# Kernel tuning notes

Hardware: AMD Instinct MI355X
Metric: run time of the kernel (lower is better)

## Reference

```python
import jax, jax.numpy as jnp
import numpy as np

B, D, CTX, H = 8192, 64, 256, 512  # batch, latent dim (made.nin), context dim, MADE hidden


def _masks(D, H):
    """Standard MADE natural-ordering masks (Germain et al. 2015)."""
    m0 = np.arange(1, D + 1)                 # input degrees 1..D
    mh = (np.arange(H) % (D - 1)) + 1        # hidden degrees 1..D-1
    M1 = (mh[:, None] >= m0[None, :]).astype(np.float32)   # (H, D)
    M2 = (mh[:, None] >= mh[None, :]).astype(np.float32)   # (H, H)
    mo = np.concatenate([m0, m0])            # outputs = [means; pre_scales]
    Mo = (mo[:, None] > mh[None, :]).astype(np.float32)    # (2D, H)
    return jnp.asarray(M1), jnp.asarray(M2), jnp.asarray(Mo)


def setup_inputs() -> dict:
    key = jax.random.key(0)
    ks = jax.random.split(key, 7)
    s = 0.05
    return {
        "context": jax.random.normal(ks[0], (B, CTX), jnp.float32),
        "eps": jax.random.normal(ks[1], (B, D), jnp.float32),  # reparameterization noise
        "W1": jax.random.normal(ks[2], (H, D), jnp.float32) * s,
        "b1": jnp.zeros((H,), jnp.float32),
        "Wc": jax.random.normal(ks[3], (H, CTX), jnp.float32) * s,
        "W2": jax.random.normal(ks[4], (H, H), jnp.float32) * s,
        "b2": jnp.zeros((H,), jnp.float32),
        "Wo": jax.random.normal(ks[5], (2 * D, H), jnp.float32) * s,
        "bo": jnp.zeros((2 * D,), jnp.float32),
    }


def reference(context, eps, W1, b1, Wc, W2, b2, Wo, bo):
    """AutoRegressiveDistribution.rsample (gaussian): D sequential MADE forwards,
    each extracting column i of (mu, softplus(pre_scale)) and sampling z_i."""
    M1, M2, Mo = _masks(D, H)
    W1m, W2m, Wom = (W1 * M1).T, (W2 * M2).T, (Wo * Mo).T
    ctx_h = context @ Wc.T  # context projection is constant across steps

    def step(z, i):
        h = jax.nn.relu(z @ W1m + ctx_h + b1)   # (B, H)
        h = jax.nn.relu(h @ W2m + b2)           # (B, H)
        out = h @ Wom + bo                      # (B, 2D): [means | pre_scales]
        mu_i = out[:, i]
        scale_i = jax.nn.softplus(out[:, D + i])
        z_i = mu_i + scale_i * eps[:, i]        # Normal(mu, scale).rsample()
        z = z.at[:, i].set(z_i)
        return z, (mu_i, scale_i)

    z0 = jnp.zeros((context.shape[0], D), context.dtype)
    z, (mus, scales) = jax.lax.scan(step, z0, jnp.arange(D))
    # state = (z_sample, mu_inferred, scale_inferred), each (B, D)
    return z, mus.T, scales.T
```

## Files before the change

### kernel.cpp

```cpp
#include <hip/hip_runtime.h>
#include <math.h>


typedef float f2 __attribute__((ext_vector_type(2)));

#define Bn 8192
#define Dn 64
#define CTXn 256
#define Hn 512
#define Rn 16

#define WQ_SZ  (64 * 512 * 12)
#define WOQ_SZ (64 * 64 * 20)
#define WCP_SZ (CTXn * Hn)

#define BARRIER() do {                                      \
    asm volatile("s_waitcnt lgkmcnt(0)" ::: "memory");      \
    __builtin_amdgcn_s_barrier();                           \
    asm volatile("" ::: "memory");                          \
  } while (0)

__device__ __forceinline__ int perm_of(int p, int* degout) {
  int k, t;
  if (p < 72) { k = p / 9 + 1; t = p - (k - 1) * 9; }
  else        { int pp = p - 72; k = pp / 8 + 9; t = pp - (k - 9) * 8; }
  *degout = k;
  return (k - 1) + 63 * t;
}
__device__ __forceinline__ int inv_perm(int h) {
  int i = h % 63;
  int t = h / 63;
  int base = (i < 9) ? 9 * i : 72 + 8 * (i - 8);
  return base + t;
}

#define R0e 262144
#define R1e (R0e + 32768)
#define R2e (R1e + 65536)
#define R3e (R2e + 131072)
#define R4e (R3e + 35840)
#define R5e (R4e + 1024)
__global__ void prep_kernel(const float* __restrict__ W1, const float* __restrict__ Wc,
                            const float* __restrict__ W2, const float* __restrict__ Wo,
                            const float* __restrict__ b1, const float* __restrict__ b2,
                            float* __restrict__ Wq, float* __restrict__ Woq,
                            float* __restrict__ WcpT, float* __restrict__ b1p,
                            float* __restrict__ b2p) {
  int idx = blockIdx.x * 256 + threadIdx.x;
  if (idx < R0e) {
    int hq = idx >> 9, hp = idx & 511;
    int i = hp % 63, e = hp / 63;
    Wq[i * 6144 + inv_perm(hq) * 12 + e] = W2[idx];
  } else if (idx < R1e) {
    int jj = idx - R0e;
    int hq = jj >> 6, i = jj & 63;
    Wq[i * 6144 + inv_perm(hq) * 12 + 9] = W1[jj];
  } else if (idx < R2e) {
    int jj = idx - R1e;
    int o = jj >> 9, hp = jj & 511;
    int i = hp % 63, p = hp / 63;
    int j = o & 63, half = o >> 6;
    Woq[i * 1280 + j * 20 + half * 10 + p] = Wo[jj];
  } else if (idx < R3e) {
    int jj = idx - R2e;
    int hq = jj >> 8, cc = jj & 255;
    int p = inv_perm(hq);
    int slot = (p < 256) ? (2 * p) : (2 * (p - 256) + 1);
    WcpT[cc * 512 + slot] = Wc[jj];
  } else if (idx < R4e) {
    int z = idx - R3e;
    if (z < 28672) {
      int i = 8 + (z >> 9), q = z & 511;
      Wq[i * 6144 + q * 12 + 8] = 0.f;
    } else {
      int z2 = z - 28672;
      int i = 8 + (z2 >> 7), r = z2 & 127;
      int j = r & 63, half = r >> 6;
      Woq[i * 1280 + j * 20 + half * 10 + 8] = 0.f;
    }
  } else if (idx < R5e) {
    int z = idx - R4e;
    if (z < 512) {
      int dq; int hq = perm_of(z, &dq);
      b1p[z] = b1[hq];
    } else {
      int q = z - 512;
      int dq; int hq = perm_of(q, &dq);
      b2p[q] = b2[hq];
    }
  }
}

__global__ __launch_bounds__(256, 2)
void made_pk_kernel(
    const float* __restrict__ context, const float* __restrict__ WcpT,
    const float* __restrict__ b1p,
    const float* __restrict__ Wq, const float* __restrict__ Woq,
    const float* __restrict__ b2p, const float* __restrict__ bo,
    const float* __restrict__ eps, float* __restrict__ out) {
  __shared__ __align__(16) float ctxR[Rn][264];
  __shared__ __align__(16) float zcur[16];
  __shared__ __align__(16) float h1g[9][16];
  __shared__ __align__(16) float h2g[9][16];

  int t = threadIdx.x;
  int b0 = blockIdx.x * Rn;
  int rp = t >> 6, l = t & 63;
  int q0 = t, q1 = t + 256;

  int g0 = ((q0 < 72) ? q0 / 9 + 1 : (q0 - 72) / 8 + 9) - 1;
  int g1 = ((q1 - 72) / 8 + 9) - 1;
  int qm = t | 63;
  int gm0s = __builtin_amdgcn_readfirstlane(
      ((qm < 72) ? qm / 9 + 1 : (qm - 72) / 8 + 9) - 1);
  int gm1s = __builtin_amdgcn_readfirstlane(((qm + 256 - 72) / 8 + 9) - 1);

  #pragma unroll
  for (int r = 0; r < Rn; ++r)
    ctxR[r][t] = context[(b0 + r) * CTXn + t];
  BARRIER();

  f2 accu[16];
  {
    f2 bias = (f2){b1p[q0], b1p[q1]};
    #pragma unroll
    for (int r = 0; r < 16; ++r) accu[r] = bias;
  }
  {
    const float* wc = WcpT + 2 * t;
    #pragma clang loop unroll(disable)
    for (int c4 = 0; c4 < CTXn / 4; ++c4) {
      f2 wv0 = *(const f2*)&wc[0];
      f2 wv1 = *(const f2*)&wc[Hn];
      f2 wv2 = *(const f2*)&wc[2 * Hn];
      f2 wv3 = *(const f2*)&wc[3 * Hn];
      wc += 4 * Hn;
      #pragma unroll
      for (int hf = 0; hf < 2; ++hf) {
        float4 x[8];
        #pragma unroll
        for (int r = 0; r < 8; ++r) x[r] = *(const float4*)&ctxR[8 * hf + r][4 * c4];
        #pragma unroll
        for (int r = 0; r < 8; ++r) {
          accu[8 * hf + r] += (f2){x[r].x, x[r].x} * wv0;
          accu[8 * hf + r] += (f2){x[r].y, x[r].y} * wv1;
          accu[8 * hf + r] += (f2){x[r].z, x[r].z} * wv2;
          accu[8 * hf + r] += (f2){x[r].w, x[r].w} * wv3;
        }
      }
    }
  }

  f2 a10[8], a11[8], a20[8], a21[8];
  #pragma unroll
  for (int r2 = 0; r2 < 8; ++r2) {
    a10[r2] = (f2){accu[2 * r2].x, accu[2 * r2 + 1].x};
    a11[r2] = (f2){accu[2 * r2].y, accu[2 * r2 + 1].y};
  }
  {
    float bb0 = b2p[q0], bb1 = b2p[q1];
    #pragma unroll
    for (int r2 = 0; r2 < 8; ++r2) {
      a20[r2] = (f2){bb0, bb0};
      a21[r2] = (f2){bb1, bb1};
    }
  }

  f2 ocA[2], ocB[2];
  ocA[0] = ocA[1] = (f2){bo[l], bo[l]};
  ocB[0] = ocB[1] = (f2){bo[l + 64], bo[l + 64]};
  int r0 = b0 + 4 * rp;
  f2 ez01 = (f2){eps[(r0 + 0) * Dn + l], eps[(r0 + 1) * Dn + l]};
  f2 ez23 = (f2){eps[(r0 + 2) * Dn + l], eps[(r0 + 3) * Dn + l]};
  f2 zs01 = (f2){0.f, 0.f}, zs23 = zs01;
  f2 mus01 = zs01, mus23 = zs01, scs01 = zs01, scs23 = zs01;

  const float* wq0p = Wq + (size_t)q0 * 12;
  const float* wq1p = Wq + (size_t)q1 * 12;
  const float* wopp = Woq + (size_t)l * 20;

  #pragma clang loop unroll(disable)
  for (int i = 0; i < Dn; ++i) {
    if (l == i) {
      f2 p01 = ocB[0], p23 = ocB[1];
      float s0 = fmaxf(p01.x, 0.f) + __logf(1.f + __expf(-fabsf(p01.x)));
      float s1 = fmaxf(p01.y, 0.f) + __logf(1.f + __expf(-fabsf(p01.y)));
      float s2 = fmaxf(p23.x, 0.f) + __logf(1.f + __expf(-fabsf(p23.x)));
      float s3 = fmaxf(p23.y, 0.f) + __logf(1.f + __expf(-fabsf(p23.y)));
      f2 sc01 = (f2){s0, s1}, sc23 = (f2){s2, s3};
      f2 z01 = ocA[0] + sc01 * ez01;
      f2 z23 = ocA[1] + sc23 * ez23;
      float4 zq = {z01.x, z01.y, z23.x, z23.y};
      *(float4*)&zcur[4 * rp] = zq;
      zs01 = z01; zs23 = z23;
      mus01 = ocA[0]; mus23 = ocA[1];
      scs01 = sc01; scs23 = sc23;
    }
    BARRIER();

    int sb = (i < 8) ? 9 * i : 8 * i + 8;
    bool liveB = (i <= gm1s);
    bool liveA = (i <= gm0s);
    float4 A1c0, A1c1, A1c2, A0c0, A0c1, A0c2;
    if (liveB) {
      const float4* a4 = (const float4*)wq1p;
      A1c0 = a4[0]; A1c1 = a4[1]; A1c2 = a4[2];
      if (liveA) {
        const float4* b4 = (const float4*)wq0p;
        A0c0 = b4[0]; A0c1 = b4[1]; A0c2 = b4[2];
      }
      float4 za = *(const float4*)&zcur[0];
      float4 zb = *(const float4*)&zcur[4];
      float4 zc = *(const float4*)&zcur[8];
      float4 zd = *(const float4*)&zcur[12];
      f2 zz[8] = {(f2){za.x, za.y}, (f2){za.z, za.w},
                  (f2){zb.x, zb.y}, (f2){zb.z, zb.w},
                  (f2){zc.x, zc.y}, (f2){zc.z, zc.w},
                  (f2){zd.x, zd.y}, (f2){zd.z, zd.w}};
      {
        f2 wv = (f2){A1c2.y, A1c2.y};
        #pragma unroll
        for (int r2 = 0; r2 < 8; ++r2) a11[r2] += wv * zz[r2];
        if (g1 == i) {
          int pp = q1 - sb;
          #pragma unroll
          for (int s = 0; s < 4; ++s) {
            float4 h = {fmaxf(a11[2 * s].x, 0.f), fmaxf(a11[2 * s].y, 0.f),
                        fmaxf(a11[2 * s + 1].x, 0.f), fmaxf(a11[2 * s + 1].y, 0.f)};
            *(float4*)&h1g[pp][4 * s] = h;
          }
        }
      }
      if (liveA) {
        f2 wv = (f2){A0c2.y, A0c2.y};
        #pragma unroll
        for (int r2 = 0; r2 < 8; ++r2) a10[r2] += wv * zz[r2];
        if (g0 == i) {
          int pp = q0 - sb;
          #pragma unroll
          for (int s = 0; s < 4; ++s) {
            float4 h = {fmaxf(a10[2 * s].x, 0.f), fmaxf(a10[2 * s].y, 0.f),
                        fmaxf(a10[2 * s + 1].x, 0.f), fmaxf(a10[2 * s + 1].y, 0.f)};
            *(float4*)&h1g[pp][4 * s] = h;
          }
        }
      }
    }
    BARRIER();

    const float4* w4 = (const float4*)wopp;
    float4 B0 = w4[0], B1 = w4[1], B2_ = w4[2], B3 = w4[3], B4 = w4[4];

    if (liveB) {
      float wA1[9] = {A1c0.x, A1c0.y, A1c0.z, A1c0.w,
                      A1c1.x, A1c1.y, A1c1.z, A1c1.w, A1c2.x};
      if (liveA) {
        float wA0[9] = {A0c0.x, A0c0.y, A0c0.z, A0c0.w,
                        A0c1.x, A0c1.y, A0c1.z, A0c1.w, A0c2.x};
        #pragma unroll
        for (int p = 0; p < 9; ++p) {
          float4 ha = *(const float4*)&h1g[p][0];
          float4 hb = *(const float4*)&h1g[p][4];
          float4 hc = *(const float4*)&h1g[p][8];
          float4 hd = *(const float4*)&h1g[p][12];
          f2 h[8] = {(f2){ha.x, ha.y}, (f2){ha.z, ha.w},
                     (f2){hb.x, hb.y}, (f2){hb.z, hb.w},
                     (f2){hc.x, hc.y}, (f2){hc.z, hc.w},
                     (f2){hd.x, hd.y}, (f2){hd.z, hd.w}};
          f2 wv1 = (f2){wA1[p], wA1[p]};
          f2 wv0 = (f2){wA0[p], wA0[p]};
          #pragma unroll
          for (int r2 = 0; r2 < 8; ++r2) {
            a21[r2] += wv1 * h[r2];
            a20[r2] += wv0 * h[r2];
          }
        }
      } else {
        #pragma unroll
        for (int p = 0; p < 9; ++p) {
          float4 ha = *(const float4*)&h1g[p][0];
          float4 hb = *(const float4*)&h1g[p][4];
          float4 hc = *(const float4*)&h1g[p][8];
          float4 hd = *(const float4*)&h1g[p][12];
          f2 h[8] = {(f2){ha.x, ha.y}, (f2){ha.z, ha.w},
                     (f2){hb.x, hb.y}, (f2){hb.z, hb.w},
                     (f2){hc.x, hc.y}, (f2){hc.z, hc.w},
                     (f2){hd.x, hd.y}, (f2){hd.z, hd.w}};
          f2 wv1 = (f2){wA1[p], wA1[p]};
          #pragma unroll
          for (int r2 = 0; r2 < 8; ++r2) a21[r2] += wv1 * h[r2];
        }
      }
      if (g1 == i) {
        int pp = q1 - sb;
        #pragma unroll
        for (int s = 0; s < 4; ++s) {
          float4 h = {fmaxf(a21[2 * s].x, 0.f), fmaxf(a21[2 * s].y, 0.f),
                      fmaxf(a21[2 * s + 1].x, 0.f), fmaxf(a21[2 * s + 1].y, 0.f)};
          *(float4*)&h2g[pp][4 * s] = h;
        }
      }
      if (liveA && g0 == i) {
        int pp = q0 - sb;
        #pragma unroll
        for (int s = 0; s < 4; ++s) {
          float4 h = {fmaxf(a20[2 * s].x, 0.f), fmaxf(a20[2 * s].y, 0.f),
                      fmaxf(a20[2 * s + 1].x, 0.f), fmaxf(a20[2 * s + 1].y, 0.f)};
          *(float4*)&h2g[pp][4 * s] = h;
        }
      }
    }
    BARRIER();

    {
      float wBa[9] = {B0.x, B0.y, B0.z, B0.w, B1.x, B1.y, B1.z, B1.w, B2_.x};
      float wBb[9] = {B2_.z, B2_.w, B3.x, B3.y, B3.z, B3.w, B4.x, B4.y, B4.z};
      #pragma unroll
      for (int p = 0; p < 9; ++p) {
        float4 hq = *(const float4*)&h2g[p][4 * rp];
        f2 h01 = (f2){hq.x, hq.y}, h23 = (f2){hq.z, hq.w};
        f2 wa = (f2){wBa[p], wBa[p]}, wb = (f2){wBb[p], wBb[p]};
        ocA[0] += wa * h01; ocA[1] += wa * h23;
        ocB[0] += wb * h01; ocB[1] += wb * h23;
      }
    }
    wq0p += 6144; wq1p += 6144; wopp += 1280;
  }

  out[(r0 + 0) * Dn + l] = zs01.x;
  out[(r0 + 1) * Dn + l] = zs01.y;
  out[(r0 + 2) * Dn + l] = zs23.x;
  out[(r0 + 3) * Dn + l] = zs23.y;
  out[Bn * Dn + (r0 + 0) * Dn + l] = mus01.x;
  out[Bn * Dn + (r0 + 1) * Dn + l] = mus01.y;
  out[Bn * Dn + (r0 + 2) * Dn + l] = mus23.x;
  out[Bn * Dn + (r0 + 3) * Dn + l] = mus23.y;
  out[2 * Bn * Dn + (r0 + 0) * Dn + l] = scs01.x;
  out[2 * Bn * Dn + (r0 + 1) * Dn + l] = scs01.y;
  out[2 * Bn * Dn + (r0 + 2) * Dn + l] = scs23.x;
  out[2 * Bn * Dn + (r0 + 3) * Dn + l] = scs23.y;
}

extern "C" void kernel_launch(void* const* d_in, const int* in_sizes, int n_in,
                              void* d_out, int out_size, void* d_ws, size_t ws_size,
                              hipStream_t stream) {
  const float* context = (const float*)d_in[0];
  const float* eps     = (const float*)d_in[1];
  const float* W1      = (const float*)d_in[2];
  const float* b1      = (const float*)d_in[3];
  const float* Wc      = (const float*)d_in[4];
  const float* W2      = (const float*)d_in[5];
  const float* b2      = (const float*)d_in[6];
  const float* Wo      = (const float*)d_in[7];
  const float* bo      = (const float*)d_in[8];
  float* out = (float*)d_out;

  float* ws   = (float*)d_ws;
  float* Wq   = ws;
  float* Woq  = Wq + WQ_SZ;
  float* WcpT = Woq + WOQ_SZ;
  float* b1p  = WcpT + WCP_SZ;
  float* b2p  = b1p + 512;

  prep_kernel<<<(R5e + 255) / 256, 256, 0, stream>>>(
      W1, Wc, W2, Wo, b1, b2, Wq, Woq, WcpT, b1p, b2p);
  made_pk_kernel<<<Bn / Rn, 256, 0, stream>>>(context, WcpT, b1p, Wq, Woq,
                                              b2p, bo, eps, out);
}
```

Measured before the change: 237.2 us.

## Software-pipeline MADE step: finish owning group per wave, defer bulk updates a step

```diff
diff --git a/kernel.cpp b/kernel.cpp
--- a/kernel.cpp
+++ b/kernel.cpp
@@ -9,6 +9,7 @@
 #define CTXn 256
 #define Hn 512
 #define Rn 16
+#define BD (Bn * Dn)
 
 #define WQ_SZ  (64 * 512 * 12)
 #define WOQ_SZ (64 * 64 * 20)
@@ -18,6 +19,10 @@
     asm volatile("s_waitcnt lgkmcnt(0)" ::: "memory");      \
     __builtin_amdgcn_s_barrier();                           \
     asm volatile("" ::: "memory");                          \
+  } while (0)
+
+#define WAVE_LDS_FENCE() do {                               \
+    asm volatile("s_waitcnt lgkmcnt(0)" ::: "memory");      \
   } while (0)
 
 __device__ __forceinline__ int perm_of(int p, int* degout) {
@@ -99,9 +104,9 @@
     const float* __restrict__ b2p, const float* __restrict__ bo,
     const float* __restrict__ eps, float* __restrict__ out) {
   __shared__ __align__(16) float ctxR[Rn][264];
-  __shared__ __align__(16) float zcur[16];
-  __shared__ __align__(16) float h1g[9][16];
-  __shared__ __align__(16) float h2g[9][16];
+  __shared__ __align__(16) float zpub[2][16];
+  __shared__ __align__(16) float h1pub[2][9][16];
+  __shared__ __align__(16) float h2pub[2][9][16];
 
   int t = threadIdx.x;
   int b0 = blockIdx.x * Rn;
@@ -150,7 +155,6 @@
       }
     }
   }
-
   f2 a10[8], a11[8], a20[8], a21[8];
   #pragma unroll
   for (int r2 = 0; r2 < 8; ++r2) {
@@ -165,7 +169,6 @@
       a21[r2] = (f2){bb1, bb1};
     }
   }
-
   f2 ocA[2], ocB[2];
   ocA[0] = ocA[1] = (f2){bo[l], bo[l]};
   ocB[0] = ocB[1] = (f2){bo[l + 64], bo[l + 64]};
@@ -175,13 +178,39 @@
   f2 zs01 = (f2){0.f, 0.f}, zs23 = zs01;
   f2 mus01 = zs01, mus23 = zs01, scs01 = zs01, scs23 = zs01;
 
-  const float* wq0p = Wq + (size_t)q0 * 12;
-  const float* wq1p = Wq + (size_t)q1 * 12;
-  const float* wopp = Woq + (size_t)l * 20;
+  float4 C1c0, C1c1, C1c2, C0c0, C0c1, C0c2;
 
   #pragma clang loop unroll(disable)
-  for (int i = 0; i < Dn; ++i) {
-    if (l == i) {
+  for (int S = 0; S < Dn; ++S) {
+    float4 P1c0, P1c1, P1c2, P0c0, P0c1, P0c2;
+    bool pldB = (S <= gm1s);
+    bool pldA = (S <= gm0s);
+    if (pldB) {
+      const float4* a4 = (const float4*)(Wq + (size_t)S * 6144 + (size_t)q1 * 12);
+      P1c0 = a4[0]; P1c1 = a4[1]; P1c2 = a4[2];
+      if (pldA) {
+        const float4* b4 = (const float4*)(Wq + (size_t)S * 6144 + (size_t)q0 * 12);
+        P0c0 = b4[0]; P0c1 = b4[1]; P0c2 = b4[2];
+      }
+    }
+
+    if (S >= 1) {
+      int i = S - 1, pb = i & 1;
+      const float4* w4 = (const float4*)(Woq + (size_t)i * 1280 + (size_t)l * 20);
+      float4 B0 = w4[0], B1 = w4[1], B2_ = w4[2], B3 = w4[3], B4 = w4[4];
+      float wBa[9] = {B0.x, B0.y, B0.z, B0.w, B1.x, B1.y, B1.z, B1.w, B2_.x};
+      float wBb[9] = {B2_.z, B2_.w, B3.x, B3.y, B3.z, B3.w, B4.x, B4.y, B4.z};
+      #pragma unroll
+      for (int p = 0; p < 9; ++p) {
+        float4 hq = *(const float4*)&h2pub[pb][p][4 * rp];
+        f2 h01 = (f2){hq.x, hq.y}, h23 = (f2){hq.z, hq.w};
+        f2 wa = (f2){wBa[p], wBa[p]}, wb = (f2){wBb[p], wBb[p]};
+        ocA[0] += wa * h01; ocA[1] += wa * h23;
+        ocB[0] += wb * h01; ocB[1] += wb * h23;
+      }
+    }
+
+    if (l == S) {
       f2 p01 = ocB[0], p23 = ocB[1];
       float s0 = fmaxf(p01.x, 0.f) + __logf(1.f + __expf(-fabsf(p01.x)));
       float s1 = fmaxf(p01.y, 0.f) + __logf(1.f + __expf(-fabsf(p01.y)));
@@ -190,155 +219,194 @@
       f2 sc01 = (f2){s0, s1}, sc23 = (f2){s2, s3};
       f2 z01 = ocA[0] + sc01 * ez01;
       f2 z23 = ocA[1] + sc23 * ez23;
-      float4 zq = {z01.x, z01.y, z23.x, z23.y};
-      *(float4*)&zcur[4 * rp] = zq;
+      *(float4*)&zpub[S & 1][4 * rp] = (float4){z01.x, z01.y, z23.x, z23.y};
       zs01 = z01; zs23 = z23;
       mus01 = ocA[0]; mus23 = ocA[1];
       scs01 = sc01; scs23 = sc23;
     }
+
+    if (S >= 1) {
+      int i = S - 1, pb = i & 1;
+      bool liveB = (i <= gm1s);
+      bool liveA = (i <= gm0s);
+      if (liveB) {
+        float4 za = *(const float4*)&zpub[pb][0];
+        float4 zb = *(const float4*)&zpub[pb][4];
+        float4 zc = *(const float4*)&zpub[pb][8];
+        float4 zd = *(const float4*)&zpub[pb][12];
+        f2 zz[8] = {(f2){za.x, za.y}, (f2){za.z, za.w},
+                    (f2){zb.x, zb.y}, (f2){zb.z, zb.w},
+                    (f2){zc.x, zc.y}, (f2){zc.z, zc.w},
+                    (f2){zd.x, zd.y}, (f2){zd.z, zd.w}};
+        {
+          f2 wv = (f2){C1c2.y, C1c2.y};
+          #pragma unroll
+          for (int r2 = 0; r2 < 8; ++r2) a11[r2] += wv * zz[r2];
+        }
+        if (liveA) {
+          f2 wv = (f2){C0c2.y, C0c2.y};
+          #pragma unroll
+          for (int r2 = 0; r2 < 8; ++r2) a10[r2] += wv * zz[r2];
+        }
+        float wA1[9] = {C1c0.x, C1c0.y, C1c0.z, C1c0.w,
+                        C1c1.x, C1c1.y, C1c1.z, C1c1.w, C1c2.x};
+        if (liveA) {
+          float wA0[9] = {C0c0.x, C0c0.y, C0c0.z, C0c0.w,
+                          C0c1.x, C0c1.y, C0c1.z, C0c1.w, C0c2.x};
+          #pragma unroll
+          for (int p = 0; p < 9; ++p) {
+            float4 ha = *(const float4*)&h1pub[pb][p][0];
+            float4 hb = *(const float4*)&h1pub[pb][p][4];
+            float4 hc = *(const float4*)&h1pub[pb][p][8];
+            float4 hd = *(const float4*)&h1pub[pb][p][12];
+            f2 h[8] = {(f2){ha.x, ha.y}, (f2){ha.z, ha.w},
+                       (f2){hb.x, hb.y}, (f2){hb.z, hb.w},
+                       (f2){hc.x, hc.y}, (f2){hc.z, hc.w},
+                       (f2){hd.x, hd.y}, (f2){hd.z, hd.w}};
+            f2 wv1 = (f2){wA1[p], wA1[p]};
+            f2 wv0 = (f2){wA0[p], wA0[p]};
+            #pragma unroll
+            for (int r2 = 0; r2 < 8; ++r2) {
+              a21[r2] += wv1 * h[r2];
+              a20[r2] += wv0 * h[r2];
+            }
+          }
+        } else {
+          #pragma unroll
+          for (int p = 0; p < 9; ++p) {
+            float4 ha = *(const float4*)&h1pub[pb][p][0];
+            float4 hb = *(const float4*)&h1pub[pb][p][4];
+            float4 hc = *(const float4*)&h1pub[pb][p][8];
+            float4 hd = *(const float4*)&h1pub[pb][p][12];
+            f2 h[8] = {(f2){ha.x, ha.y}, (f2){ha.z, ha.w},
+                       (f2){hb.x, hb.y}, (f2){hb.z, hb.w},
+                       (f2){hc.x, hc.y}, (f2){hc.z, hc.w},
+                       (f2){hd.x, hd.y}, (f2){hd.z, hd.w}};
+            f2 wv1 = (f2){wA1[p], wA1[p]};
+            #pragma unroll
+            for (int r2 = 0; r2 < 8; ++r2) a21[r2] += wv1 * h[r2];
+          }
+        }
+      }
+    }
     BARRIER();
 
-    int sb = (i < 8) ? 9 * i : 8 * i + 8;
-    bool liveB = (i <= gm1s);
-    bool liveA = (i <= gm0s);
-    float4 A1c0, A1c1, A1c2, A0c0, A0c1, A0c2;
-    if (liveB) {
-      const float4* a4 = (const float4*)wq1p;
-      A1c0 = a4[0]; A1c1 = a4[1]; A1c2 = a4[2];
-      if (liveA) {
-        const float4* b4 = (const float4*)wq0p;
-        A0c0 = b4[0]; A0c1 = b4[1]; A0c2 = b4[2];
-      }
-      float4 za = *(const float4*)&zcur[0];
-      float4 zb = *(const float4*)&zcur[4];
-      float4 zc = *(const float4*)&zcur[8];
-      float4 zd = *(const float4*)&zcur[12];
+    int ps = S & 1;
+    int sb = (S < 8) ? 9 * S : 8 * S + 8;
+    bool fin1 = (g1 == S);
+    bool fin0 = (g0 == S);
+    if (fin1) {
+      float4 za = *(const float4*)&zpub[ps][0];
+      float4 zb = *(const float4*)&zpub[ps][4];
+      float4 zc = *(const float4*)&zpub[ps][8];
+      float4 zd = *(const float4*)&zpub[ps][12];
       f2 zz[8] = {(f2){za.x, za.y}, (f2){za.z, za.w},
                   (f2){zb.x, zb.y}, (f2){zb.z, zb.w},
                   (f2){zc.x, zc.y}, (f2){zc.z, zc.w},
                   (f2){zd.x, zd.y}, (f2){zd.z, zd.w}};
-      {
-        f2 wv = (f2){A1c2.y, A1c2.y};
+      f2 wv = (f2){P1c2.y, P1c2.y};
+      #pragma unroll
+      for (int r2 = 0; r2 < 8; ++r2) a11[r2] += wv * zz[r2];
+      int pp = q1 - sb;
+      #pragma unroll
+      for (int s = 0; s < 4; ++s) {
+        *(float4*)&h1pub[ps][pp][4 * s] =
+            (float4){fmaxf(a11[2 * s].x, 0.f), fmaxf(a11[2 * s].y, 0.f),
+                     fmaxf(a11[2 * s + 1].x, 0.f), fmaxf(a11[2 * s + 1].y, 0.f)};
+      }
+    }
+    if (fin0) {
+      float4 za = *(const float4*)&zpub[ps][0];
+      float4 zb = *(const float4*)&zpub[ps][4];
+      float4 zc = *(const float4*)&zpub[ps][8];
+      float4 zd = *(const float4*)&zpub[ps][12];
+      f2 zz[8] = {(f2){za.x, za.y}, (f2){za.z, za.w},
+                  (f2){zb.x, zb.y}, (f2){zb.z, zb.w},
+                  (f2){zc.x, zc.y}, (f2){zc.z, zc.w},
+                  (f2){zd.x, zd.y}, (f2){zd.z, zd.w}};
+      f2 wv = (f2){P0c2.y, P0c2.y};
+      #pragma unroll
+      for (int r2 = 0; r2 < 8; ++r2) a10[r2] += wv * zz[r2];
+      int pp = q0 - sb;
+      #pragma unroll
+      for (int s = 0; s < 4; ++s) {
+        *(float4*)&h1pub[ps][pp][4 * s] =
+            (float4){fmaxf(a10[2 * s].x, 0.f), fmaxf(a10[2 * s].y, 0.f),
+                     fmaxf(a10[2 * s + 1].x, 0.f), fmaxf(a10[2 * s + 1].y, 0.f)};
+      }
+    }
+    WAVE_LDS_FENCE();
+    if (S == 7) BARRIER();
+    if (fin1) {
+      float wc[9] = {P1c0.x, P1c0.y, P1c0.z, P1c0.w,
+                     P1c1.x, P1c1.y, P1c1.z, P1c1.w, P1c2.x};
+      #pragma unroll
+      for (int k = 0; k < 9; ++k) {
+        float4 ha = *(const float4*)&h1pub[ps][k][0];
+        float4 hb = *(const float4*)&h1pub[ps][k][4];
+        float4 hc = *(const float4*)&h1pub[ps][k][8];
+        float4 hd = *(const float4*)&h1pub[ps][k][12];
+        f2 h[8] = {(f2){ha.x, ha.y}, (f2){ha.z, ha.w},
+                   (f2){hb.x, hb.y}, (f2){hb.z, hb.w},
+                   (f2){hc.x, hc.y}, (f2){hc.z, hc.w},
+                   (f2){hd.x, hd.y}, (f2){hd.z, hd.w}};
+        f2 wv = (f2){wc[k], wc[k]};
         #pragma unroll
-        for (int r2 = 0; r2 < 8; ++r2) a11[r2] += wv * zz[r2];
-        if (g1 == i) {
-          int pp = q1 - sb;
-          #pragma unroll
-          for (int s = 0; s < 4; ++s) {
-            float4 h = {fmaxf(a11[2 * s].x, 0.f), fmaxf(a11[2 * s].y, 0.f),
-                        fmaxf(a11[2 * s + 1].x, 0.f), fmaxf(a11[2 * s + 1].y, 0.f)};
-            *(float4*)&h1g[pp][4 * s] = h;
-          }
-        }
-      }
-      if (liveA) {
-        f2 wv = (f2){A0c2.y, A0c2.y};
+        for (int r2 = 0; r2 < 8; ++r2) a21[r2] += wv * h[r2];
+      }
+      int pp = q1 - sb;
+      #pragma unroll
+      for (int s = 0; s < 4; ++s) {
+        *(float4*)&h2pub[ps][pp][4 * s] =
+            (float4){fmaxf(a21[2 * s].x, 0.f), fmaxf(a21[2 * s].y, 0.f),
+                     fmaxf(a21[2 * s + 1].x, 0.f), fmaxf(a21[2 * s + 1].y, 0.f)};
+      }
+    }
+    if (fin0) {
+      float wc[9] = {P0c0.x, P0c0.y, P0c0.z, P0c0.w,
+                     P0c1.x, P0c1.y, P0c1.z, P0c1.w, P0c2.x};
+      #pragma unroll
+      for (int k = 0; k < 9; ++k) {
+        float4 ha = *(const float4*)&h1pub[ps][k][0];
+        float4 hb = *(const float4*)&h1pub[ps][k][4];
+        float4 hc = *(const float4*)&h1pub[ps][k][8];
+        float4 hd = *(const float4*)&h1pub[ps][k][12];
+        f2 h[8] = {(f2){ha.x, ha.y}, (f2){ha.z, ha.w},
+                   (f2){hb.x, hb.y}, (f2){hb.z, hb.w},
+                   (f2){hc.x, hc.y}, (f2){hc.z, hc.w},
+                   (f2){hd.x, hd.y}, (f2){hd.z, hd.w}};
+        f2 wv = (f2){wc[k], wc[k]};
         #pragma unroll
-        for (int r2 = 0; r2 < 8; ++r2) a10[r2] += wv * zz[r2];
-        if (g0 == i) {
-          int pp = q0 - sb;
-          #pragma unroll
-          for (int s = 0; s < 4; ++s) {
-            float4 h = {fmaxf(a10[2 * s].x, 0.f), fmaxf(a10[2 * s].y, 0.f),
-                        fmaxf(a10[2 * s + 1].x, 0.f), fmaxf(a10[2 * s + 1].y, 0.f)};
-            *(float4*)&h1g[pp][4 * s] = h;
-          }
-        }
+        for (int r2 = 0; r2 < 8; ++r2) a20[r2] += wv * h[r2];
+      }
+      int pp = q0 - sb;
+      #pragma unroll
+      for (int s = 0; s < 4; ++s) {
+        *(float4*)&h2pub[ps][pp][4 * s] =
+            (float4){fmaxf(a20[2 * s].x, 0.f), fmaxf(a20[2 * s].y, 0.f),
+                     fmaxf(a20[2 * s + 1].x, 0.f), fmaxf(a20[2 * s + 1].y, 0.f)};
       }
     }
     BARRIER();
 
-    const float4* w4 = (const float4*)wopp;
-    float4 B0 = w4[0], B1 = w4[1], B2_ = w4[2], B3 = w4[3], B4 = w4[4];
-
-    if (liveB) {
-      float wA1[9] = {A1c0.x, A1c0.y, A1c0.z, A1c0.w,
-                      A1c1.x, A1c1.y, A1c1.z, A1c1.w, A1c2.x};
-      if (liveA) {
-        float wA0[9] = {A0c0.x, A0c0.y, A0c0.z, A0c0.w,
-                        A0c1.x, A0c1.y, A0c1.z, A0c1.w, A0c2.x};
-        #pragma unroll
-        for (int p = 0; p < 9; ++p) {
-          float4 ha = *(const float4*)&h1g[p][0];
-          float4 hb = *(const float4*)&h1g[p][4];
-          float4 hc = *(const float4*)&h1g[p][8];
-          float4 hd = *(const float4*)&h1g[p][12];
-          f2 h[8] = {(f2){ha.x, ha.y}, (f2){ha.z, ha.w},
-                     (f2){hb.x, hb.y}, (f2){hb.z, hb.w},
-                     (f2){hc.x, hc.y}, (f2){hc.z, hc.w},
-                     (f2){hd.x, hd.y}, (f2){hd.z, hd.w}};
-          f2 wv1 = (f2){wA1[p], wA1[p]};
-          f2 wv0 = (f2){wA0[p], wA0[p]};
-          #pragma unroll
-          for (int r2 = 0; r2 < 8; ++r2) {
-            a21[r2] += wv1 * h[r2];
-            a20[r2] += wv0 * h[r2];
-          }
-        }
-      } else {
-        #pragma unroll
-        for (int p = 0; p < 9; ++p) {
-          float4 ha = *(const float4*)&h1g[p][0];
-          float4 hb = *(const float4*)&h1g[p][4];
-          float4 hc = *(const float4*)&h1g[p][8];
-          float4 hd = *(const float4*)&h1g[p][12];
-          f2 h[8] = {(f2){ha.x, ha.y}, (f2){ha.z, ha.w},
-                     (f2){hb.x, hb.y}, (f2){hb.z, hb.w},
-                     (f2){hc.x, hc.y}, (f2){hc.z, hc.w},
-                     (f2){hd.x, hd.y}, (f2){hd.z, hd.w}};
-          f2 wv1 = (f2){wA1[p], wA1[p]};
-          #pragma unroll
-          for (int r2 = 0; r2 < 8; ++r2) a21[r2] += wv1 * h[r2];
-        }
-      }
-      if (g1 == i) {
-        int pp = q1 - sb;
-        #pragma unroll
-        for (int s = 0; s < 4; ++s) {
-          float4 h = {fmaxf(a21[2 * s].x, 0.f), fmaxf(a21[2 * s].y, 0.f),
-                      fmaxf(a21[2 * s + 1].x, 0.f), fmaxf(a21[2 * s + 1].y, 0.f)};
-          *(float4*)&h2g[pp][4 * s] = h;
-        }
-      }
-      if (liveA && g0 == i) {
-        int pp = q0 - sb;
-        #pragma unroll
-        for (int s = 0; s < 4; ++s) {
-          float4 h = {fmaxf(a20[2 * s].x, 0.f), fmaxf(a20[2 * s].y, 0.f),
-                      fmaxf(a20[2 * s + 1].x, 0.f), fmaxf(a20[2 * s + 1].y, 0.f)};
-          *(float4*)&h2g[pp][4 * s] = h;
-        }
-      }
-    }
-    BARRIER();
-
-    {
-      float wBa[9] = {B0.x, B0.y, B0.z, B0.w, B1.x, B1.y, B1.z, B1.w, B2_.x};
-      float wBb[9] = {B2_.z, B2_.w, B3.x, B3.y, B3.z, B3.w, B4.x, B4.y, B4.z};
-      #pragma unroll
-      for (int p = 0; p < 9; ++p) {
-        float4 hq = *(const float4*)&h2g[p][4 * rp];
-        f2 h01 = (f2){hq.x, hq.y}, h23 = (f2){hq.z, hq.w};
-        f2 wa = (f2){wBa[p], wBa[p]}, wb = (f2){wBb[p], wBb[p]};
-        ocA[0] += wa * h01; ocA[1] += wa * h23;
-        ocB[0] += wb * h01; ocB[1] += wb * h23;
-      }
-    }
-    wq0p += 6144; wq1p += 6144; wopp += 1280;
+    if (pldB) {
+      C1c0 = P1c0; C1c1 = P1c1; C1c2 = P1c2;
+      if (pldA) { C0c0 = P0c0; C0c1 = P0c1; C0c2 = P0c2; }
+    }
   }
 
   out[(r0 + 0) * Dn + l] = zs01.x;
   out[(r0 + 1) * Dn + l] = zs01.y;
   out[(r0 + 2) * Dn + l] = zs23.x;
   out[(r0 + 3) * Dn + l] = zs23.y;
-  out[Bn * Dn + (r0 + 0) * Dn + l] = mus01.x;
-  out[Bn * Dn + (r0 + 1) * Dn + l] = mus01.y;
-  out[Bn * Dn + (r0 + 2) * Dn + l] = mus23.x;
-  out[Bn * Dn + (r0 + 3) * Dn + l] = mus23.y;
-  out[2 * Bn * Dn + (r0 + 0) * Dn + l] = scs01.x;
-  out[2 * Bn * Dn + (r0 + 1) * Dn + l] = scs01.y;
-  out[2 * Bn * Dn + (r0 + 2) * Dn + l] = scs23.x;
-  out[2 * Bn * Dn + (r0 + 3) * Dn + l] = scs23.y;
+  out[BD + (r0 + 0) * Dn + l] = mus01.x;
+  out[BD + (r0 + 1) * Dn + l] = mus01.y;
+  out[BD + (r0 + 2) * Dn + l] = mus23.x;
+  out[BD + (r0 + 3) * Dn + l] = mus23.y;
+  out[2 * BD + (r0 + 0) * Dn + l] = scs01.x;
+  out[2 * BD + (r0 + 1) * Dn + l] = scs01.y;
+  out[2 * BD + (r0 + 2) * Dn + l] = scs23.x;
+  out[2 * BD + (r0 + 3) * Dn + l] = scs23.y;
 }
 
 extern "C" void kernel_launch(void* const* d_in, const int* in_sizes, int n_in,
```

Result: slower. 264.8 us (+11.6%).
